# Kernel optimization log

Measured on AMD Instinct MI355X. Metric: run time of the kernel, lower is better.

The kernel has to match this reference:

```python
import jax, jax.numpy as jnp
import numpy as np

RESO = 64
VSIZE = 0.3
VOXEL = VSIZE / RESO
HALF = VOXEL / 2.0


def _voxel_xyz():
    line = (np.arange(RESO, dtype=np.float32) * VOXEL + HALF)
    x, y, z = np.meshgrid(line, line, line, indexing='ij')
    return jnp.asarray(np.stack([x, y, z]))  # [3,R,R,R]


def _grid_sample_2d(feats, gx, gy):
    # feats: [NV,C,H,W]; gx,gy: [NV,N] normalized coords (torch align_corners-style)
    NV, C, H, W = feats.shape
    ix = (gx + 1.0) * 0.5 * (W - 1)
    iy = (gy + 1.0) * 0.5 * (H - 1)
    ix0 = jnp.floor(ix); iy0 = jnp.floor(iy)
    ix1 = ix0 + 1.0;     iy1 = iy0 + 1.0
    # bilinear weights from unclamped corners
    w_nw = (ix1 - ix) * (iy1 - iy)
    w_ne = (ix - ix0) * (iy1 - iy)
    w_sw = (ix1 - ix) * (iy - iy0)
    w_se = (ix - ix0) * (iy - iy0)
    mask = ((ix >= 0) & (ix <= W - 1) & (iy >= 0) & (iy <= H - 1)).astype(feats.dtype)
    cx0 = jnp.clip(ix0, 0, W - 1).astype(jnp.int32)
    cx1 = jnp.clip(ix1, 0, W - 1).astype(jnp.int32)
    cy0 = jnp.clip(iy0, 0, H - 1).astype(jnp.int32)
    cy1 = jnp.clip(iy1, 0, H - 1).astype(jnp.int32)
    feats_flat = feats.reshape(NV, C, H * W)  # [NV,C,HW]
    gather = jax.vmap(lambda f, i: f[:, i])   # per-view [C,HW],[N] -> [C,N]
    v_nw = gather(feats_flat, cy0 * W + cx0)
    v_ne = gather(feats_flat, cy0 * W + cx1)
    v_sw = gather(feats_flat, cy1 * W + cx0)
    v_se = gather(feats_flat, cy1 * W + cx1)
    out = (v_nw * w_nw[:, None] + v_ne * w_ne[:, None]
           + v_sw * w_sw[:, None] + v_se * w_se[:, None])  # [NV,C,N]
    return out, mask


def setup_inputs() -> dict:
    key = jax.random.key(0)
    k_feat, k1, k2, k3 = jax.random.split(key, 4)
    NV, C, H, W = 8, 32, 128, 128
    feats = jax.random.normal(k_feat, (NV, C, H, W), dtype=jnp.float32)
    # realistic pinhole intrinsics for a 512x512 image
    K = np.array([[400.0, 0.0, 256.0], [0.0, 400.0, 256.0], [0.0, 0.0, 1.0]], np.float32)
    Ks = jnp.asarray(np.tile(K, (NV, 1, 1)))
    # identity-rotation w2c poses, camera ~0.5m from volume along +z
    poses = []
    for i in range(NV):
        t = np.array([0.02 * (i - 3.5), 0.01 * (i % 2), 0.5 + 0.02 * i], np.float32)
        poses.append(np.concatenate([np.eye(3, dtype=np.float32), t[:, None]], axis=1))
    ref_poses = jnp.asarray(np.stack(poses))
    bbox = jnp.asarray(np.array([[-0.15, -0.15, 0.0], [0.15, 0.15, 0.3]], np.float32))
    W1 = jax.random.normal(k1, (32, 32), dtype=jnp.float32) * 0.1
    W2 = jax.random.normal(k2, (32, 16), dtype=jnp.float32) * 0.1
    W3 = jax.random.normal(k3, (16, 8), dtype=jnp.float32) * 0.1
    return {"feats": feats, "ref_poses": ref_poses, "Ks": Ks, "bbox": bbox,
            "img_h": 512, "img_w": 512,
            "W1": W1, "b1": jnp.zeros((32,), jnp.float32),
            "W2": W2, "b2": jnp.zeros((16,), jnp.float32),
            "W3": W3, "b3": jnp.zeros((8,), jnp.float32)}


def reference(feats, ref_poses, Ks, bbox, img_h, img_w, W1, b1, W2, b2, W3, b3):
    NV, C, H, W = feats.shape
    dt = feats.dtype
    # homogeneous pad of poses and intrinsics
    pose_h = jnp.tile(jnp.eye(4, dtype=dt), (NV, 1, 1)).at[:, :3, :4].set(ref_poses)
    K_pad = jnp.tile(jnp.eye(4, dtype=dt), (NV, 1, 1)).at[:, :3, :3].set(Ks)
    w2pixel = K_pad @ pose_h  # [NV,4,4]
    # voxel centers in world frame
    xyz = _voxel_xyz() + bbox[0][:, None, None, None]  # [3,R,R,R]
    pts = xyz.reshape(3, -1)                            # [3,N], N=R^3
    homo = jnp.concatenate([pts, jnp.ones_like(pts[0:1])], axis=0)  # [4,N]
    pix = jnp.einsum('vij,jn->vin', w2pixel, homo)[:, :3]           # [NV,3,N]
    z = pix[:, 2]                                                    # [NV,N]
    mask_valid_depth = (z > 0).astype(dt)
    uv = pix[:, :2] / z[:, None, :]                                  # [NV,2,N]
    normalizer = jnp.array([img_w, img_h], dtype=dt)
    grid = uv.transpose(0, 2, 1) / normalizer - 1.0                  # [NV,N,2]
    feat, mask = _grid_sample_2d(feats, grid[..., 0], grid[..., 1])  # [NV,C,N],[NV,N]
    mask = mask * mask_valid_depth
    # [NV,C,(X Y Z)] -> [NV,X,Y,Z,C]
    feat = feat.transpose(0, 2, 1).reshape(NV, RESO, RESO, RESO, C)
    mask = mask.reshape(NV, RESO, RESO, RESO)
    # NOTE: original normalizes over dim=1 (NumX), replicated faithfully
    weight = mask / (jnp.sum(mask, axis=1, keepdims=True) + 1e-8)
    weight = weight[..., None]  # [NV,R,R,R,1]
    h1 = jax.nn.relu(feat @ W1 + b1)
    h2 = jax.nn.relu(h1 @ W2 + b2)
    comp = h2 @ W3 + b3  # [NV,R,R,R,8]
    mean = jnp.sum(comp * weight, axis=0, keepdims=True)
    var = jnp.sum(weight * (comp - mean) ** 2, axis=0, keepdims=True)
    mv = jnp.concatenate([mean, var], axis=-1)       # [1,R,R,R,16]
    return jnp.transpose(mv, (0, 4, 3, 2, 1))        # [1,16,Z,Y,X]
```

## Files before the change

kernel.cpp:

```cpp
#include <hip/hip_runtime.h>
#include <math.h>

#define NVIEW 8
#define CIN   32
#define HF    128
#define WF    128
#define C1    32
#define C2    16
#define C3    8
#define RESO  64
#define PLANE (HF*WF)

typedef _Float16 half8_t  __attribute__((ext_vector_type(8)));
typedef _Float16 half2_t  __attribute__((ext_vector_type(2)));
typedef float    floatx4  __attribute__((ext_vector_type(4)));

static __device__ __forceinline__ float vox_coord(int idx, float b) {
    const float VOXEL = (float)(0.3 / 64.0);
    const float HALFV = (float)(0.3 / 128.0);
    return (float)idx * VOXEL + HALFV + b;
}

static __device__ __forceinline__ void wave_lds_sync() {
    asm volatile("s_waitcnt lgkmcnt(0)" ::: "memory");
}

__global__ void __launch_bounds__(256) k_g(const float* __restrict__ feats,
                                           const float* __restrict__ W1,
                                           const float* __restrict__ b1,
                                           uint4* __restrict__ Gh,
                                           const float* __restrict__ Ks,
                                           const float* __restrict__ poses,
                                           const int* __restrict__ ihp,
                                           const int* __restrict__ iwp,
                                           const float* __restrict__ W2,
                                           const float* __restrict__ b2,
                                           const float* __restrict__ W3,
                                           const float* __restrict__ b3,
                                           float* __restrict__ mats,
                                           _Float16* __restrict__ w2f,
                                           _Float16* __restrict__ w3f,
                                           float* __restrict__ b2f,
                                           float* __restrict__ b3f) {
    if (blockIdx.x == 512) {
        int t = threadIdx.x;
        if (t < NVIEW * 12) {
            int v = t / 12, rc = t % 12, r = rc / 4, c = rc % 4;
            const float* K = Ks + v * 9;
            const float* P = poses + v * 12;
            float s = K[r*3+0]*P[0*4+c] + K[r*3+1]*P[1*4+c] + K[r*3+2]*P[2*4+c];
            float sc = (r == 0) ? 63.5f / (float)iwp[0]
                     : (r == 1) ? 63.5f / (float)ihp[0] : 1.0f;
            mats[v*12 + r*4 + c] = s * sc;
        }
        if (t < 64) {
            int n = t & 15, g = t >> 4;
#pragma unroll
            for (int jj = 0; jj < 8; jj++) {
                int kk = 8 * g + jj;
                w2f[t*8 + jj] = (_Float16)W2[kk * C2 + n];
                float w3v = (kk < C2 && n < C3) ? W3[kk * C3 + n] : 0.0f;
                w3f[t*8 + jj] = (_Float16)w3v;
            }
            b2f[t] = b2[n];
            b3f[t] = (n < C3) ? b3[n] : 0.0f;
        }
        return;
    }
    int bx = blockIdx.x;
    int pix = (bx & 63) * 256 + threadIdx.x;
    int v   = bx >> 6;
    const float* fp = feats + ((size_t)v * CIN) * PLANE + pix;
    float g[32];
#pragma unroll
    for (int o = 0; o < C1; o++) g[o] = b1[o];
#pragma unroll
    for (int cc = 0; cc < CIN; cc += 8) {
        float fc[8];
#pragma unroll
        for (int q = 0; q < 8; q++) fc[q] = fp[(size_t)(cc + q) * PLANE];
#pragma unroll
        for (int q = 0; q < 8; q++) {
#pragma unroll
            for (int o = 0; o < C1; o++)
                g[o] = fmaf(fc[q], W1[(cc + q) * C1 + o], g[o]);
        }
    }
#pragma unroll
    for (int grp = 0; grp < 4; grp++) {
        union { half2_t h2[4]; uint4 u; } pk;
#pragma unroll
        for (int q = 0; q < 4; q++) {
            half2_t p = { (_Float16)g[grp*8 + 2*q], (_Float16)g[grp*8 + 2*q + 1] };
            pk.h2[q] = p;
        }
        Gh[((size_t)(v * 4 + grp)) * PLANE + pix] = pk.u;
    }
}

__global__ void __launch_bounds__(256) k_main(
    const uint4* __restrict__ Gh,
    const float* __restrict__ mats, const float* __restrict__ bbox,
    const _Float16* __restrict__ w2f, const _Float16* __restrict__ w3f,
    const float* __restrict__ b2f, const float* __restrict__ b3f,
    float* __restrict__ out) {
#pragma clang fp contract(fast)
    __shared__ __align__(16) _Float16 h2s[4][64 * 24];

    int tid  = threadIdx.x;
    int wv   = tid >> 6;
    int lane = tid & 63;
    int bx   = (blockIdx.x & 7) * 128 + (blockIdx.x >> 3);
    int col  = bx * 4 + wv;
    int j  = col & 63;
    int kz = col >> 6;
    _Float16* h2b = h2s[wv];

    int m = lane & 15, g = lane >> 4;
    float y = vox_coord(j, bbox[1]);
    float z = vox_coord(kz, bbox[2]);

    half8_t w2frag = *(const half8_t*)(w2f + lane * 8);
    half8_t w3frag = *(const half8_t*)(w3f + lane * 8);
    float b2c = b2f[lane];
    float b3c = b3f[lane];
    floatx4 cb2 = {b2c, b2c, b2c, b2c};
    floatx4 cb3 = {b3c, b3c, b3c, b3c};
    const half2_t z2 = { (_Float16)0.0f, (_Float16)0.0f };

    float M1[16], Msq[16], S16[16];
#pragma unroll
    for (int c = 0; c < 16; c++) { M1[c] = 0.0f; Msq[c] = 0.0f; S16[c] = 0.0f; }

#pragma unroll 2
    for (int v = 0; v < NVIEW; v++) {
        const float* M = mats + v * 12;
        const uint4* Gv = Gh + (size_t)(v * 4 + g) * PLANE;

        float Ku = fmaf(M[1], y, fmaf(M[2],  z, M[3]));
        float Kv = fmaf(M[5], y, fmaf(M[6],  z, M[7]));
        float Kz = fmaf(M[9], y, fmaf(M[10], z, M[11]));
        float M0 = M[0], M4 = M[4], M8 = M[8];

        floatx4 c2v[4];
        unsigned int ballo[4];
        int popc = 0;

#pragma unroll
        for (int T = 0; T < 4; T++) {
            int ipt = T * 16 + m;
            float x = vox_coord(ipt, bbox[0]);
            float u  = fmaf(M0, x, Ku);
            float vv = fmaf(M4, x, Kv);
            float zc = fmaf(M8, x, Kz);
            float invz = __builtin_amdgcn_rcpf(zc);
            float ix = u * invz;
            float iy = vv * invz;

            float fx0 = floorf(ix), fy0 = floorf(iy);
            float fx1 = fx0 + 1.0f, fy1 = fy0 + 1.0f;
            bool inb = (ix >= 0.0f) && (ix <= (float)(WF-1)) &&
                       (iy >= 0.0f) && (iy <= (float)(HF-1)) && (zc > 0.0f);
            int cx0 = (int)fminf(fmaxf(fx0, 0.0f), (float)(WF-1));
            int cx1 = (int)fminf(fmaxf(fx1, 0.0f), (float)(WF-1));
            int cy0 = (int)fminf(fmaxf(fy0, 0.0f), (float)(HF-1));
            int cy1 = (int)fminf(fmaxf(fy1, 0.0f), (float)(HF-1));
            float wnw = (fx1 - ix) * (fy1 - iy);
            float wne = (ix - fx0) * (fy1 - iy);
            float wsw = (fx1 - ix) * (iy - fy0);
            float wse = (ix - fx0) * (iy - fy0);

            unsigned long long bal = __ballot(inb);
            ballo[T] = (unsigned int)bal;
            popc += __popcll(bal);

            int t00 = cy0 * WF + cx0, t01 = cy0 * WF + cx1;
            int t10 = cy1 * WF + cx0, t11 = cy1 * WF + cx1;
            uint4 A = Gv[t00], B = Gv[t01], C = Gv[t10], D = Gv[t11];

            half2_t wnw2 = { (_Float16)wnw, (_Float16)wnw };
            half2_t wne2 = { (_Float16)wne, (_Float16)wne };
            half2_t wsw2 = { (_Float16)wsw, (_Float16)wsw };
            half2_t wse2 = { (_Float16)wse, (_Float16)wse };

            union { uint4 u; half2_t h[4]; } ua, ub, uc, ud;
            ua.u = A; ub.u = B; uc.u = C; ud.u = D;
            union { half2_t h2[4]; half8_t h8; } r;
#pragma unroll
            for (int c = 0; c < 4; c++) {
                half2_t e = ua.h[c]*wnw2 + ub.h[c]*wne2 + uc.h[c]*wsw2 + ud.h[c]*wse2;
                r.h2[c] = __builtin_elementwise_max(e, z2);
            }

            c2v[T] = __builtin_amdgcn_mfma_f32_16x16x32_f16(r.h8, w2frag, cb2, 0, 0, 0);
        }

        wave_lds_sync();
#pragma unroll
        for (int T = 0; T < 4; T++) {
#pragma unroll
            for (int r = 0; r < 4; r++) {
                float vv = fmaxf(c2v[T][r], 0.0f);
                h2b[(T*16 + g*4 + r) * 24 + m] = (_Float16)vv;
            }
        }
        wave_lds_sync();

        float msr = __builtin_amdgcn_rcpf((float)(popc >> 2) + 1e-8f);
#pragma unroll
        for (int T = 0; T < 4; T++) {
            half8_t a3 = *(const half8_t*)(h2b + (T*16 + m) * 24 + (g & 1) * 8);
            floatx4 c3 = __builtin_amdgcn_mfma_f32_16x16x32_f16(a3, w3frag, cb3, 0, 0, 0);
#pragma unroll
            for (int r = 0; r < 4; r++) {
                float w = ((ballo[T] >> (g*4 + r)) & 1u) ? msr : 0.0f;
                float val = c3[r];
                float t1 = w * val;
                S16[T*4+r] += w;
                M1[T*4+r]  += t1;
                Msq[T*4+r]  = fmaf(t1, val, Msq[T*4+r]);
            }
        }
    }

    if (m < C3) {
        size_t base = (size_t)col * 64;
#pragma unroll
        for (int T = 0; T < 4; T++) {
            float4 mn, vr;
            mn.x = M1[T*4+0]; mn.y = M1[T*4+1]; mn.z = M1[T*4+2]; mn.w = M1[T*4+3];
            vr.x = fmaf(mn.x*mn.x, S16[T*4+0]-2.0f, Msq[T*4+0]);
            vr.y = fmaf(mn.y*mn.y, S16[T*4+1]-2.0f, Msq[T*4+1]);
            vr.z = fmaf(mn.z*mn.z, S16[T*4+2]-2.0f, Msq[T*4+2]);
            vr.w = fmaf(mn.w*mn.w, S16[T*4+3]-2.0f, Msq[T*4+3]);
            size_t ob = base + T*16 + g*4;
            *(float4*)(out + (size_t)m       * 262144 + ob) = mn;
            *(float4*)(out + (size_t)(m + 8) * 262144 + ob) = vr;
        }
    }
}

extern "C" void kernel_launch(void* const* d_in, const int* in_sizes, int n_in,
                              void* d_out, int out_size, void* d_ws, size_t ws_size,
                              hipStream_t stream) {
    const float* feats = (const float*)d_in[0];
    const float* poses = (const float*)d_in[1];
    const float* Ks    = (const float*)d_in[2];
    const float* bbox  = (const float*)d_in[3];
    const int*   img_h = (const int*)d_in[4];
    const int*   img_w = (const int*)d_in[5];
    const float* W1    = (const float*)d_in[6];
    const float* b1    = (const float*)d_in[7];
    const float* W2    = (const float*)d_in[8];
    const float* b2    = (const float*)d_in[9];
    const float* W3    = (const float*)d_in[10];
    const float* b3    = (const float*)d_in[11];
    float* out = (float*)d_out;
    float* ws  = (float*)d_ws;

    float*     mats = ws;
    _Float16*  w2f  = (_Float16*)(ws + 128);
    _Float16*  w3f  = (_Float16*)(ws + 384);
    float*     b2f  = ws + 640;
    float*     b3f  = ws + 704;
    uint4*     Gh   = (uint4*)(ws + 768);

    hipLaunchKernelGGL(k_g, dim3(513), dim3(256), 0, stream,
                       feats, W1, b1, Gh, Ks, poses, img_h, img_w,
                       W2, b2, W3, b3, mats, w2f, w3f, b2f, b3f);
    hipLaunchKernelGGL(k_main, dim3(1024), dim3(256), 0, stream,
                       Gh, mats, bbox, w2f, w3f, b2f, b3f, out);
}
```

Before: 131.9 us.

## Software-pipeline bilinear gathers across views to overlap loads with compute

The per-view loop is restructured so the four bilinear corner gathers for view v+1 are issued while view v's blend and MFMA work is being consumed, with ballots and counts double-buffered by view parity. The loop is fully unrolled. The aim is to hide global/L2 gather latency behind the MFMA, LDS and reduction work of the previous view. In exchange, register pressure rises from holding 16 uint4 gathered values plus weights across iterations, which may reduce occupancy or cause spills.

```diff
diff --git a/kernel.cpp b/kernel.cpp
--- a/kernel.cpp
+++ b/kernel.cpp
@@ -110,13 +110,14 @@
     int tid  = threadIdx.x;
     int wv   = tid >> 6;
     int lane = tid & 63;
-    int bx   = (blockIdx.x & 7) * 128 + (blockIdx.x >> 3);
-    int col  = bx * 4 + wv;
+    int bxs  = (blockIdx.x & 7) * 128 + (blockIdx.x >> 3);
+    int col  = bxs * 4 + wv;
     int j  = col & 63;
     int kz = col >> 6;
     _Float16* h2b = h2s[wv];
 
     int m = lane & 15, g = lane >> 4;
+    float b0 = bbox[0];
     float y = vox_coord(j, bbox[1]);
     float z = vox_coord(kz, bbox[2]);
 
@@ -132,68 +133,90 @@
 #pragma unroll
     for (int c = 0; c < 16; c++) { M1[c] = 0.0f; Msq[c] = 0.0f; S16[c] = 0.0f; }
 
-#pragma unroll 2
+    uint4 gA[4], gB[4], gC[4], gD[4];
+    half2_t w4[4][4];
+    unsigned int ball2[2][4];
+    int pcnt2[2];
+    float vKu, vKv, vKz, vM0, vM4, vM8;
+    const uint4* vGv;
+
+#define VSETUP(vv) do {                                                  \
+        const float* Mv_ = mats + (vv) * 12;                             \
+        vKu = fmaf(Mv_[1], y, fmaf(Mv_[2],  z, Mv_[3]));                 \
+        vKv = fmaf(Mv_[5], y, fmaf(Mv_[6],  z, Mv_[7]));                 \
+        vKz = fmaf(Mv_[9], y, fmaf(Mv_[10], z, Mv_[11]));                \
+        vM0 = Mv_[0]; vM4 = Mv_[4]; vM8 = Mv_[8];                        \
+        vGv = Gh + (size_t)((vv) * 4 + g) * PLANE;                       \
+    } while (0)
+
+#define ISSUE(T, VPAR) do {                                              \
+        int ipt_ = (T) * 16 + m;                                         \
+        float x_ = vox_coord(ipt_, b0);                                  \
+        float u_  = fmaf(vM0, x_, vKu);                                  \
+        float vv_ = fmaf(vM4, x_, vKv);                                  \
+        float zc_ = fmaf(vM8, x_, vKz);                                  \
+        float invz_ = __builtin_amdgcn_rcpf(zc_);                        \
+        float ix_ = u_ * invz_;                                          \
+        float iy_ = vv_ * invz_;                                         \
+        float fx0_ = floorf(ix_), fy0_ = floorf(iy_);                    \
+        float fx1_ = fx0_ + 1.0f, fy1_ = fy0_ + 1.0f;                    \
+        bool inb_ = (ix_ >= 0.0f) && (ix_ <= (float)(WF-1)) &&           \
+                    (iy_ >= 0.0f) && (iy_ <= (float)(HF-1)) && (zc_ > 0.0f); \
+        int cx0_ = (int)fminf(fmaxf(fx0_, 0.0f), (float)(WF-1));         \
+        int cx1_ = (int)fminf(fmaxf(fx1_, 0.0f), (float)(WF-1));         \
+        int cy0_ = (int)fminf(fmaxf(fy0_, 0.0f), (float)(HF-1));         \
+        int cy1_ = (int)fminf(fmaxf(fy1_, 0.0f), (float)(HF-1));         \
+        float wnw_ = (fx1_ - ix_) * (fy1_ - iy_);                        \
+        float wne_ = (ix_ - fx0_) * (fy1_ - iy_);                        \
+        float wsw_ = (fx1_ - ix_) * (iy_ - fy0_);                        \
+        float wse_ = (ix_ - fx0_) * (iy_ - fy0_);                        \
+        unsigned long long bal_ = __ballot(inb_);                        \
+        ball2[VPAR][T] = (unsigned int)bal_;                             \
+        pcnt2[VPAR] += __popcll(bal_);                                   \
+        int t00_ = cy0_ * WF + cx0_, t01_ = cy0_ * WF + cx1_;            \
+        int t10_ = cy1_ * WF + cx0_, t11_ = cy1_ * WF + cx1_;            \
+        gA[T] = vGv[t00_]; gB[T] = vGv[t01_];                            \
+        gC[T] = vGv[t10_]; gD[T] = vGv[t11_];                            \
+        half2_t wnw2_ = { (_Float16)wnw_, (_Float16)wnw_ };    \
+        half2_t wne2_ = { (_Float16)wne_, (_Float16)wne_ };              \
+        half2_t wsw2_ = { (_Float16)wsw_, (_Float16)wsw_ };              \
+        half2_t wse2_ = { (_Float16)wse_, (_Float16)wse_ };              \
+        w4[T][0] = wnw2_; w4[T][1] = wne2_;                              \
+        w4[T][2] = wsw2_; w4[T][3] = wse2_;                              \
+    } while (0)
+
+#define CONSUME(T) do {                                                  \
+        union { uint4 u; half2_t h[4]; } ua_, ub_, uc_, ud_;             \
+        ua_.u = gA[T]; ub_.u = gB[T]; uc_.u = gC[T]; ud_.u = gD[T];      \
+        union { half2_t h2[4]; half8_t h8; } r_;                         \
+        _Pragma("unroll")                                                \
+        for (int c_ = 0; c_ < 4; c_++) {                                 \
+            half2_t e_ = ua_.h[c_]*w4[T][0] + ub_.h[c_]*w4[T][1]         \
+                       + uc_.h[c_]*w4[T][2] + ud_.h[c_]*w4[T][3];        \
+            r_.h2[c_] = __builtin_elementwise_max(e_, z2);     \
+        }                                                                \
+        c2v[T] = __builtin_amdgcn_mfma_f32_16x16x32_f16(r_.h8, w2frag, cb2, 0, 0, 0); \
+    } while (0)
+
+    floatx4 c2v[4];
+
+    VSETUP(0);
+    pcnt2[0] = 0;
+    ISSUE(0, 0); ISSUE(1, 0); ISSUE(2, 0); ISSUE(3, 0);
+
+#pragma unroll
     for (int v = 0; v < NVIEW; v++) {
-        const float* M = mats + v * 12;
-        const uint4* Gv = Gh + (size_t)(v * 4 + g) * PLANE;
-
-        float Ku = fmaf(M[1], y, fmaf(M[2],  z, M[3]));
-        float Kv = fmaf(M[5], y, fmaf(M[6],  z, M[7]));
-        float Kz = fmaf(M[9], y, fmaf(M[10], z, M[11]));
-        float M0 = M[0], M4 = M[4], M8 = M[8];
-
-        floatx4 c2v[4];
-        unsigned int ballo[4];
-        int popc = 0;
-
-#pragma unroll
-        for (int T = 0; T < 4; T++) {
-            int ipt = T * 16 + m;
-            float x = vox_coord(ipt, bbox[0]);
-            float u  = fmaf(M0, x, Ku);
-            float vv = fmaf(M4, x, Kv);
-            float zc = fmaf(M8, x, Kz);
-            float invz = __builtin_amdgcn_rcpf(zc);
-            float ix = u * invz;
-            float iy = vv * invz;
-
-            float fx0 = floorf(ix), fy0 = floorf(iy);
-            float fx1 = fx0 + 1.0f, fy1 = fy0 + 1.0f;
-            bool inb = (ix >= 0.0f) && (ix <= (float)(WF-1)) &&
-                       (iy >= 0.0f) && (iy <= (float)(HF-1)) && (zc > 0.0f);
-            int cx0 = (int)fminf(fmaxf(fx0, 0.0f), (float)(WF-1));
-            int cx1 = (int)fminf(fmaxf(fx1, 0.0f), (float)(WF-1));
-            int cy0 = (int)fminf(fmaxf(fy0, 0.0f), (float)(HF-1));
-            int cy1 = (int)fminf(fmaxf(fy1, 0.0f), (float)(HF-1));
-            float wnw = (fx1 - ix) * (fy1 - iy);
-            float wne = (ix - fx0) * (fy1 - iy);
-            float wsw = (fx1 - ix) * (iy - fy0);
-            float wse = (ix - fx0) * (iy - fy0);
-
-            unsigned long long bal = __ballot(inb);
-            ballo[T] = (unsigned int)bal;
-            popc += __popcll(bal);
-
-            int t00 = cy0 * WF + cx0, t01 = cy0 * WF + cx1;
-            int t10 = cy1 * WF + cx0, t11 = cy1 * WF + cx1;
-            uint4 A = Gv[t00], B = Gv[t01], C = Gv[t10], D = Gv[t11];
-
-            half2_t wnw2 = { (_Float16)wnw, (_Float16)wnw };
-            half2_t wne2 = { (_Float16)wne, (_Float16)wne };
-            half2_t wsw2 = { (_Float16)wsw, (_Float16)wsw };
-            half2_t wse2 = { (_Float16)wse, (_Float16)wse };
-
-            union { uint4 u; half2_t h[4]; } ua, ub, uc, ud;
-            ua.u = A; ub.u = B; uc.u = C; ud.u = D;
-            union { half2_t h2[4]; half8_t h8; } r;
-#pragma unroll
-            for (int c = 0; c < 4; c++) {
-                half2_t e = ua.h[c]*wnw2 + ub.h[c]*wne2 + uc.h[c]*wsw2 + ud.h[c]*wse2;
-                r.h2[c] = __builtin_elementwise_max(e, z2);
-            }
-
-            c2v[T] = __builtin_amdgcn_mfma_f32_16x16x32_f16(r.h8, w2frag, cb2, 0, 0, 0);
-        }
+        const int vp = v & 1;
+        const int np = (v + 1) & 1;
+
+        CONSUME(0);
+        if (v < NVIEW - 1) { VSETUP(v + 1); pcnt2[np] = 0; ISSUE(0, np); }
+        CONSUME(1);
+        if (v < NVIEW - 1) ISSUE(1, np);
+        CONSUME(2);
+        if (v < NVIEW - 1) ISSUE(2, np);
+        CONSUME(3);
+        if (v < NVIEW - 1) ISSUE(3, np);
 
         wave_lds_sync();
 #pragma unroll
@@ -206,14 +229,14 @@
         }
         wave_lds_sync();
 
-        float msr = __builtin_amdgcn_rcpf((float)(popc >> 2) + 1e-8f);
+        float msr = __builtin_amdgcn_rcpf((float)(pcnt2[vp] >> 2) + 1e-8f);
 #pragma unroll
         for (int T = 0; T < 4; T++) {
             half8_t a3 = *(const half8_t*)(h2b + (T*16 + m) * 24 + (g & 1) * 8);
             floatx4 c3 = __builtin_amdgcn_mfma_f32_16x16x32_f16(a3, w3frag, cb3, 0, 0, 0);
 #pragma unroll
             for (int r = 0; r < 4; r++) {
-                float w = ((ballo[T] >> (g*4 + r)) & 1u) ? msr : 0.0f;
+                float w = ((ball2[vp][T] >> (g*4 + r)) & 1u) ? msr : 0.0f;
                 float val = c3[r];
                 float t1 = w * val;
                 S16[T*4+r] += w;
@@ -222,6 +245,10 @@
             }
         }
     }
+
+#undef VSETUP
+#undef ISSUE
+#undef CONSUME
 
     if (m < C3) {
         size_t base = (size_t)col * 64;
```

New measurement: 135.7 us. 2.9% more time.
